# Optimization experiments

Measured on AMD Instinct MI355X. Metric: run time of the kernel, lower is better.

## Reference

```python
import jax, jax.numpy as jnp
import numpy as np

N, L, H, E = 4, 4096, 8, 64
CHUNK = 128  # chunk size for the blocked causal scan
EPS = 1e-6


def elu_feature_map(x):
    # phi(x) = elu(x) + 1 (default feature map of fast-transformers)
    return jax.nn.elu(x) + 1.0


def causal_dot_product(Q, K, V, chunk=CHUNK):
    """out[n,l,h,:] = sum_{s<=l} (Q[n,l,h,:].K[n,s,h,:]) * V[n,s,h,:].
    Chunked scan over the [E,M] KV state: O(N L H E M) without an [L,L] matrix."""
    n, l, h, e = Q.shape
    m = V.shape[-1]
    nc = l // chunk

    def to_chunks(x):
        # [n, l, h, d] -> [nc, n, h, chunk, d]
        return x.reshape(n, nc, chunk, h, x.shape[-1]).transpose(1, 0, 3, 2, 4)

    q, k, v = to_chunks(Q), to_chunks(K), to_chunks(V)
    tril = jnp.tril(jnp.ones((chunk, chunk), dtype=Q.dtype))

    def step(S, xs):  # S: [n, h, e, m] running sum of k v^T
        qc, kc, vc = xs  # [n, h, chunk, e/m]
        inter = jnp.einsum('nhce,nhem->nhcm', qc, S)
        attn = jnp.einsum('nhce,nhde->nhcd', qc, kc) * tril  # intra-chunk causal
        intra = jnp.einsum('nhcd,nhdm->nhcm', attn, vc)
        S = S + jnp.einsum('nhce,nhcm->nhem', kc, vc)
        return S, inter + intra

    S0 = jnp.zeros((n, h, e, m), dtype=Q.dtype)
    _, out = jax.lax.scan(step, S0, (q, k, v))  # [nc, n, h, chunk, m]
    return out.transpose(1, 0, 3, 2, 4).reshape(n, l, h, m)


def setup_inputs() -> dict:
    key = jax.random.key(0)
    k1, k2, k3 = jax.random.split(key, 3)
    return {
        'queries': jax.random.normal(k1, (N, L, H, E), jnp.float32),
        'keys': jax.random.normal(k2, (N, L, H, E), jnp.float32),
        'values': jax.random.normal(k3, (N, L, H, E), jnp.float32),
        'key_lengths': jnp.ones((N, L), jnp.float32),  # float length mask
    }


def reference(queries, keys, values, key_lengths):
    Q = elu_feature_map(queries)
    K = elu_feature_map(keys) * key_lengths[:, :, None, None]
    # denominator: Z[n,l,h] = 1 / (Q[n,l,h] . cumsum_s<=l K[n,s,h] + eps)
    Z = 1.0 / (jnp.einsum('nlhe,nlhe->nlh', Q, jnp.cumsum(K, axis=1)) + EPS)
    V_new = causal_dot_product(Q, K, values)
    return V_new * Z[:, :, :, None]
```

## Files before the change

kernel.cpp:

```cpp
#include <hip/hip_runtime.h>
#include <math.h>

#define NN 4
#define LL 4096
#define HH 8
#define EE 64
#define CHK 64
#define NCH (LL/CHK)
#define NG (NN*HH*NCH)
#define EPSF 1e-6f

typedef float f32x4 __attribute__((ext_vector_type(4)));
typedef __bf16 bf16x8 __attribute__((ext_vector_type(8)));

__device__ __forceinline__ float phi_map(float x) {
  return x > 0.0f ? x + 1.0f : __expf(x);
}

#define MFMA(a, b, c) __builtin_amdgcn_mfma_f32_16x16x32_bf16((a), (b), (c), 0, 0, 0)

__device__ __forceinline__ int swz64(int row, int d) {
  return row * 64 + (d & 7) + 8 * ((d >> 3) ^ ((row >> 2) & 7));
}
__device__ __forceinline__ int frag64(int row, int blk) {
  return row * 64 + 8 * (blk ^ ((row >> 2) & 7));
}

__global__ __launch_bounds__(256) void k_chunksums(
    const float* __restrict__ Kg, const float* __restrict__ Vg,
    const float* __restrict__ KLg, __bf16* __restrict__ ScG, __bf16* __restrict__ KscG)
{
  __shared__ __bf16 sKt[4096];
  __shared__ __bf16 sVt[4096];
  const int g = blockIdx.x;
  const int c = g % NCH;
  const int nh = g / NCH;
  const int h = nh % HH;
  const int n = nh / HH;
  const int l0 = c * CHK;
  const int t = threadIdx.x;

  #pragma unroll
  for (int it = 0; it < 4; ++it) {
    int f = t + 256 * it;
    int d = f >> 4;
    int c4 = (f & 15) << 2;
    size_t gb = (((size_t)n * LL + (size_t)(l0 + d)) * HH + h) * EE + c4;
    float4 kk = *(const float4*)(Kg + gb);
    float4 vv = *(const float4*)(Vg + gb);
    float klr = KLg[n * LL + l0 + d];
    float ka[4] = {phi_map(kk.x) * klr, phi_map(kk.y) * klr,
                   phi_map(kk.z) * klr, phi_map(kk.w) * klr};
    float va[4] = {vv.x, vv.y, vv.z, vv.w};
    #pragma unroll
    for (int j = 0; j < 4; ++j) {
      sKt[swz64(c4 + j, d)] = (__bf16)ka[j];
      sVt[swz64(c4 + j, d)] = (__bf16)va[j];
    }
  }
  __syncthreads();

  const int w = t >> 6;
  const int lane = t & 63;
  const int lg = lane >> 4;
  const int li = lane & 15;

  bf16x8 aV[2];
  #pragma unroll
  for (int ks = 0; ks < 2; ++ks)
    aV[ks] = *(const bf16x8*)&sVt[frag64(16 * w + li, 4 * ks + lg)];

  bf16x8 ones;
  #pragma unroll
  for (int i = 0; i < 8; ++i) ones[i] = (__bf16)1.0f;

  f32x4 acc[4], accK[4];
  #pragma unroll
  for (int nt = 0; nt < 4; ++nt) {
    acc[nt] = (f32x4){0.f, 0.f, 0.f, 0.f};
    accK[nt] = (f32x4){0.f, 0.f, 0.f, 0.f};
  }

  #pragma unroll
  for (int nt = 0; nt < 4; ++nt) {
    #pragma unroll
    for (int ks = 0; ks < 2; ++ks) {
      bf16x8 b = *(const bf16x8*)&sKt[frag64(li + 16 * nt, 4 * ks + lg)];
      acc[nt] = MFMA(aV[ks], b, acc[nt]);
      if (w == 0) accK[nt] = MFMA(ones, b, accK[nt]);
    }
  }

  __bf16* sp = ScG + (size_t)g * 4096;
  #pragma unroll
  for (int nt = 0; nt < 4; ++nt)
    #pragma unroll
    for (int reg = 0; reg < 4; ++reg)
      sp[(16 * w + 4 * lg + reg) * 64 + li + 16 * nt] = (__bf16)acc[nt][reg];

  if (w == 0 && lg == 0) {
    #pragma unroll
    for (int nt = 0; nt < 4; ++nt)
      KscG[(size_t)g * 64 + li + 16 * nt] = (__bf16)accK[nt][0];
  }
}

__global__ __launch_bounds__(256) void k_prefix(
    __bf16* __restrict__ Sc, __bf16* __restrict__ Ksc)
{
  const int bid = blockIdx.x;
  const int t = threadIdx.x;
  if (bid < NN * HH * 16) {
    const int nh = bid >> 4;
    const int strip = bid & 15;
    const int entry = strip * 256 + t;
    __bf16 v[NCH];
    #pragma unroll
    for (int c = 0; c < NCH; ++c)
      v[c] = Sc[((size_t)(nh * NCH + c) << 12) + entry];
    float run = 0.0f;
    #pragma unroll
    for (int c = 0; c < NCH; ++c) {
      Sc[((size_t)(nh * NCH + c) << 12) + entry] = (__bf16)run;
      run += (float)v[c];
    }
  } else {
    const int idx = (bid - NN * HH * 16) * 256 + t;
    const int nh = idx >> 6;
    const int e = idx & 63;
    __bf16 v[NCH];
    #pragma unroll
    for (int c = 0; c < NCH; ++c)
      v[c] = Ksc[((size_t)(nh * NCH + c) << 6) + e];
    float run = 0.0f;
    #pragma unroll
    for (int c = 0; c < NCH; ++c) {
      Ksc[((size_t)(nh * NCH + c) << 6) + e] = (__bf16)run;
      run += (float)v[c];
    }
  }
}

__global__ __launch_bounds__(256, 6) void k_pass2(
    const float* __restrict__ Qg, const float* __restrict__ Kg,
    const float* __restrict__ Vg, const float* __restrict__ KLg,
    const __bf16* __restrict__ Sp, const __bf16* __restrict__ Ksp,
    float* __restrict__ Og)
{
  __shared__ __bf16 sK[64][72];
  __shared__ __bf16 sVt[4096];
  __shared__ __bf16 sU[4608];

  const int g = blockIdx.x;
  const int c = g % NCH;
  const int nh = g / NCH;
  const int h = nh % HH;
  const int n = nh / HH;
  const int t = threadIdx.x;
  const int w = t >> 6;
  const int lane = t & 63;
  const int lg = lane >> 4;
  const int li = lane & 15;
  const int l0 = c * CHK;

  {
    const bf16x8* sp8 = (const bf16x8*)(Sp + (size_t)g * 4096);
    bf16x8 s0 = sp8[2 * t];
    bf16x8 s1 = sp8[2 * t + 1];
    int m = t >> 2;
    int e0 = (t & 3) * 16;
    *(bf16x8*)&sU[m * 72 + e0] = s0;
    *(bf16x8*)&sU[m * 72 + e0 + 8] = s1;
  }

  #pragma unroll
  for (int it = 0; it < 4; ++it) {
    int f = t + 256 * it;
    int rr = f >> 4;
    int c4 = (f & 15) << 2;
    size_t gb = (((size_t)n * LL + (size_t)(l0 + rr)) * HH + h) * EE + c4;
    float4 kk = *(const float4*)(Kg + gb);
    float4 vv = *(const float4*)(Vg + gb);
    float klr = KLg[n * LL + l0 + rr];
    __bf16* kd = &sK[rr][c4];
    kd[0] = (__bf16)(phi_map(kk.x) * klr); kd[1] = (__bf16)(phi_map(kk.y) * klr);
    kd[2] = (__bf16)(phi_map(kk.z) * klr); kd[3] = (__bf16)(phi_map(kk.w) * klr);
    float va[4] = {vv.x, vv.y, vv.z, vv.w};
    #pragma unroll
    for (int j = 0; j < 4; ++j)
      sVt[swz64(c4 + j, rr)] = (__bf16)va[j];
  }

  const int arow = 16 * w + li;
  const float* qrow = Qg + (((size_t)n * LL + (size_t)(l0 + arow)) * HH + h) * EE;
  float4 q0 = *(const float4*)(qrow + 8 * lg);
  float4 q1 = *(const float4*)(qrow + 8 * lg + 4);
  float4 q2 = *(const float4*)(qrow + 32 + 8 * lg);
  float4 q3 = *(const float4*)(qrow + 32 + 8 * lg + 4);
  bf16x8 aQ0, aQ1;
  aQ0[0] = (__bf16)phi_map(q0.x); aQ0[1] = (__bf16)phi_map(q0.y);
  aQ0[2] = (__bf16)phi_map(q0.z); aQ0[3] = (__bf16)phi_map(q0.w);
  aQ0[4] = (__bf16)phi_map(q1.x); aQ0[5] = (__bf16)phi_map(q1.y);
  aQ0[6] = (__bf16)phi_map(q1.z); aQ0[7] = (__bf16)phi_map(q1.w);
  aQ1[0] = (__bf16)phi_map(q2.x); aQ1[1] = (__bf16)phi_map(q2.y);
  aQ1[2] = (__bf16)phi_map(q2.z); aQ1[3] = (__bf16)phi_map(q2.w);
  aQ1[4] = (__bf16)phi_map(q3.x); aQ1[5] = (__bf16)phi_map(q3.y);
  aQ1[6] = (__bf16)phi_map(q3.z); aQ1[7] = (__bf16)phi_map(q3.w);

  const __bf16* kb = Ksp + (size_t)g * 64;
  bf16x8 ks0 = *(const bf16x8*)(kb + 8 * lg);
  bf16x8 ks1 = *(const bf16x8*)(kb + 32 + 8 * lg);

  __syncthreads();

  f32x4 acc[4];
  #pragma unroll
  for (int nt = 0; nt < 4; ++nt) acc[nt] = (f32x4){0.f, 0.f, 0.f, 0.f};
  #pragma unroll
  for (int nt = 0; nt < 4; ++nt) {
    bf16x8 b0 = *(const bf16x8*)&sU[(li + 16 * nt) * 72 + 8 * lg];
    bf16x8 b1 = *(const bf16x8*)&sU[(li + 16 * nt) * 72 + 32 + 8 * lg];
    acc[nt] = MFMA(aQ0, b0, acc[nt]);
    acc[nt] = MFMA(aQ1, b1, acc[nt]);
  }

  float dv = 0.0f;
  #pragma unroll
  for (int i = 0; i < 8; ++i) {
    dv += (float)aQ0[i] * (float)ks0[i];
    dv += (float)aQ1[i] * (float)ks1[i];
  }
  dv += __shfl_xor(dv, 16);
  dv += __shfl_xor(dv, 32);
  float den[4];
  #pragma unroll
  for (int reg = 0; reg < 4; ++reg) den[reg] = __shfl(dv, 4 * lg + reg);

  __syncthreads();

  float rs[4] = {0.f, 0.f, 0.f, 0.f};
  #pragma unroll
  for (int nt = 0; nt < 4; ++nt) {
    f32x4 at2 = (f32x4){0.f, 0.f, 0.f, 0.f};
    if (nt <= w) {
      bf16x8 b0 = *(const bf16x8*)&sK[li + 16 * nt][8 * lg];
      bf16x8 b1 = *(const bf16x8*)&sK[li + 16 * nt][32 + 8 * lg];
      at2 = MFMA(aQ0, b0, at2);
      at2 = MFMA(aQ1, b1, at2);
    }
    #pragma unroll
    for (int reg = 0; reg < 4; ++reg) {
      int row = 16 * w + 4 * lg + reg;
      int col = li + 16 * nt;
      float av = (col <= row) ? at2[reg] : 0.0f;
      rs[reg] += av;
      sU[w * 1152 + (4 * lg + reg) * 72 + col] = (__bf16)av;
    }
  }

  {
    bf16x8 aA0 = *(const bf16x8*)&sU[w * 1152 + li * 72 + 8 * lg];
    bf16x8 aA1 = aA0;
    if (w >= 2) aA1 = *(const bf16x8*)&sU[w * 1152 + li * 72 + 32 + 8 * lg];
    #pragma unroll
    for (int nt = 0; nt < 4; ++nt) {
      bf16x8 bv0 = *(const bf16x8*)&sVt[frag64(li + 16 * nt, lg)];
      acc[nt] = MFMA(aA0, bv0, acc[nt]);
      if (w >= 2) {
        bf16x8 bv1 = *(const bf16x8*)&sVt[frag64(li + 16 * nt, 4 + lg)];
        acc[nt] = MFMA(aA1, bv1, acc[nt]);
      }
    }
  }

  #pragma unroll
  for (int reg = 0; reg < 4; ++reg) {
    float v = rs[reg];
    v += __shfl_xor(v, 1);
    v += __shfl_xor(v, 2);
    v += __shfl_xor(v, 4);
    v += __shfl_xor(v, 8);
    rs[reg] = v;
  }

  #pragma unroll
  for (int reg = 0; reg < 4; ++reg) {
    float inv = 1.0f / (den[reg] + rs[reg] + EPSF);
    int row = l0 + 16 * w + 4 * lg + reg;
    size_t ob = (((size_t)n * LL + row) * HH + h) * EE + li;
    #pragma unroll
    for (int nt = 0; nt < 4; ++nt)
      Og[ob + 16 * nt] = acc[nt][reg] * inv;
  }
}

extern "C" void kernel_launch(void* const* d_in, const int* in_sizes, int n_in,
                              void* d_out, int out_size, void* d_ws, size_t ws_size,
                              hipStream_t stream) {
  const float* Qg  = (const float*)d_in[0];
  const float* Kg  = (const float*)d_in[1];
  const float* Vg  = (const float*)d_in[2];
  const float* KLg = (const float*)d_in[3];
  float* Og = (float*)d_out;

  __bf16* Sc  = (__bf16*)d_ws;
  __bf16* Ksc = (__bf16*)((char*)d_ws + (size_t)NG * 4096 * 2);

  hipLaunchKernelGGL(k_chunksums, dim3(NG), dim3(256), 0, stream, Kg, Vg, KLg, Sc, Ksc);
  hipLaunchKernelGGL(k_prefix, dim3(NN*HH*16 + 8), dim3(256), 0, stream, Sc, Ksc);
  hipLaunchKernelGGL(k_pass2, dim3(NG), dim3(256), 0, stream, Qg, Kg, Vg, KLg, Sc, Ksc, Og);
}
```

Before: 51.34 us.

## Process four chunks per block with in-block state carry and register prefetch

Each block now handles a super-chunk of four 64-row chunks instead of one. Inside a block the KV state is carried forward with MFMA updates, so the inter-block prefix scan works on a quarter as many state entries. Global loads of the next chunk are prefetched into registers and staged into double-buffered shared memory while the current chunk computes. In exchange, blocks run a serial dependency chain, the grid is four times smaller (512 blocks), and each block uses more shared memory and registers.

```diff
diff --git a/kernel.cpp b/kernel.cpp
--- a/kernel.cpp
+++ b/kernel.cpp
@@ -6,8 +6,12 @@
 #define HH 8
 #define EE 64
 #define CHK 64
-#define NCH (LL/CHK)
-#define NG (NN*HH*NCH)
+#define GSUP 4
+#define SUPC (CHK*GSUP)
+#define NSUP (LL/SUPC)
+#define NH (NN*HH)
+#define NBLK (NH*NSUP)
+#define NCH64 (LL/CHK)
 #define EPSF 1e-6f
 
 typedef float f32x4 __attribute__((ext_vector_type(4)));
@@ -26,134 +30,34 @@
   return row * 64 + 8 * (blk ^ ((row >> 2) & 7));
 }
 
-__global__ __launch_bounds__(256) void k_chunksums(
+#define K1_ISSUE(J, BUF) { \
+  const int l0i = (sc * GSUP + (J)) * CHK; \
+  _Pragma("unroll") for (int it = 0; it < 4; ++it) { \
+    int f = t + 256 * it; int d = f >> 4; int c4 = (f & 15) << 2; \
+    size_t gb = (((size_t)n * LL + (size_t)(l0i + d)) * HH + h) * EE + c4; \
+    pk[BUF][it] = *(const float4*)(Kg + gb); \
+    pv[BUF][it] = *(const float4*)(Vg + gb); \
+    pl[BUF][it] = KLg[n * LL + l0i + d]; } }
+
+#define K1_STAGE(BUF) { \
+  _Pragma("unroll") for (int it = 0; it < 4; ++it) { \
+    int f = t + 256 * it; int d = f >> 4; int c4 = (f & 15) << 2; \
+    float klr = pl[BUF][it]; float4 kk = pk[BUF][it]; float4 vv = pv[BUF][it]; \
+    float ka[4] = {phi_map(kk.x) * klr, phi_map(kk.y) * klr, phi_map(kk.z) * klr, phi_map(kk.w) * klr}; \
+    float va[4] = {vv.x, vv.y, vv.z, vv.w}; \
+    _Pragma("unroll") for (int jj = 0; jj < 4; ++jj) { \
+      sKt[BUF][swz64(c4 + jj, d)] = (__bf16)ka[jj]; \
+      sVt[BUF][swz64(c4 + jj, d)] = (__bf16)va[jj]; } } }
+
+__global__ __launch_bounds__(256, 2) void k_chunksums(
     const float* __restrict__ Kg, const float* __restrict__ Vg,
     const float* __restrict__ KLg, __bf16* __restrict__ ScG, __bf16* __restrict__ KscG)
 {
-  __shared__ __bf16 sKt[4096];
-  __shared__ __bf16 sVt[4096];
+  __shared__ __bf16 sKt[2][4096];
+  __shared__ __bf16 sVt[2][4096];
   const int g = blockIdx.x;
-  const int c = g % NCH;
-  const int nh = g / NCH;
-  const int h = nh % HH;
-  const int n = nh / HH;
-  const int l0 = c * CHK;
-  const int t = threadIdx.x;
-
-  #pragma unroll
-  for (int it = 0; it < 4; ++it) {
-    int f = t + 256 * it;
-    int d = f >> 4;
-    int c4 = (f & 15) << 2;
-    size_t gb = (((size_t)n * LL + (size_t)(l0 + d)) * HH + h) * EE + c4;
-    float4 kk = *(const float4*)(Kg + gb);
-    float4 vv = *(const float4*)(Vg + gb);
-    float klr = KLg[n * LL + l0 + d];
-    float ka[4] = {phi_map(kk.x) * klr, phi_map(kk.y) * klr,
-                   phi_map(kk.z) * klr, phi_map(kk.w) * klr};
-    float va[4] = {vv.x, vv.y, vv.z, vv.w};
-    #pragma unroll
-    for (int j = 0; j < 4; ++j) {
-      sKt[swz64(c4 + j, d)] = (__bf16)ka[j];
-      sVt[swz64(c4 + j, d)] = (__bf16)va[j];
-    }
-  }
-  __syncthreads();
-
-  const int w = t >> 6;
-  const int lane = t & 63;
-  const int lg = lane >> 4;
-  const int li = lane & 15;
-
-  bf16x8 aV[2];
-  #pragma unroll
-  for (int ks = 0; ks < 2; ++ks)
-    aV[ks] = *(const bf16x8*)&sVt[frag64(16 * w + li, 4 * ks + lg)];
-
-  bf16x8 ones;
-  #pragma unroll
-  for (int i = 0; i < 8; ++i) ones[i] = (__bf16)1.0f;
-
-  f32x4 acc[4], accK[4];
-  #pragma unroll
-  for (int nt = 0; nt < 4; ++nt) {
-    acc[nt] = (f32x4){0.f, 0.f, 0.f, 0.f};
-    accK[nt] = (f32x4){0.f, 0.f, 0.f, 0.f};
-  }
-
-  #pragma unroll
-  for (int nt = 0; nt < 4; ++nt) {
-    #pragma unroll
-    for (int ks = 0; ks < 2; ++ks) {
-      bf16x8 b = *(const bf16x8*)&sKt[frag64(li + 16 * nt, 4 * ks + lg)];
-      acc[nt] = MFMA(aV[ks], b, acc[nt]);
-      if (w == 0) accK[nt] = MFMA(ones, b, accK[nt]);
-    }
-  }
-
-  __bf16* sp = ScG + (size_t)g * 4096;
-  #pragma unroll
-  for (int nt = 0; nt < 4; ++nt)
-    #pragma unroll
-    for (int reg = 0; reg < 4; ++reg)
-      sp[(16 * w + 4 * lg + reg) * 64 + li + 16 * nt] = (__bf16)acc[nt][reg];
-
-  if (w == 0 && lg == 0) {
-    #pragma unroll
-    for (int nt = 0; nt < 4; ++nt)
-      KscG[(size_t)g * 64 + li + 16 * nt] = (__bf16)accK[nt][0];
-  }
-}
-
-__global__ __launch_bounds__(256) void k_prefix(
-    __bf16* __restrict__ Sc, __bf16* __restrict__ Ksc)
-{
-  const int bid = blockIdx.x;
-  const int t = threadIdx.x;
-  if (bid < NN * HH * 16) {
-    const int nh = bid >> 4;
-    const int strip = bid & 15;
-    const int entry = strip * 256 + t;
-    __bf16 v[NCH];
-    #pragma unroll
-    for (int c = 0; c < NCH; ++c)
-      v[c] = Sc[((size_t)(nh * NCH + c) << 12) + entry];
-    float run = 0.0f;
-    #pragma unroll
-    for (int c = 0; c < NCH; ++c) {
-      Sc[((size_t)(nh * NCH + c) << 12) + entry] = (__bf16)run;
-      run += (float)v[c];
-    }
-  } else {
-    const int idx = (bid - NN * HH * 16) * 256 + t;
-    const int nh = idx >> 6;
-    const int e = idx & 63;
-    __bf16 v[NCH];
-    #pragma unroll
-    for (int c = 0; c < NCH; ++c)
-      v[c] = Ksc[((size_t)(nh * NCH + c) << 6) + e];
-    float run = 0.0f;
-    #pragma unroll
-    for (int c = 0; c < NCH; ++c) {
-      Ksc[((size_t)(nh * NCH + c) << 6) + e] = (__bf16)run;
-      run += (float)v[c];
-    }
-  }
-}
-
-__global__ __launch_bounds__(256, 6) void k_pass2(
-    const float* __restrict__ Qg, const float* __restrict__ Kg,
-    const float* __restrict__ Vg, const float* __restrict__ KLg,
-    const __bf16* __restrict__ Sp, const __bf16* __restrict__ Ksp,
-    float* __restrict__ Og)
-{
-  __shared__ __bf16 sK[64][72];
-  __shared__ __bf16 sVt[4096];
-  __shared__ __bf16 sU[4608];
-
-  const int g = blockIdx.x;
-  const int c = g % NCH;
-  const int nh = g / NCH;
+  const int sc = g % NSUP;
+  const int nh = g / NSUP;
   const int h = nh % HH;
   const int n = nh / HH;
   const int t = threadIdx.x;
@@ -161,7 +65,147 @@
   const int lane = t & 63;
   const int lg = lane >> 4;
   const int li = lane & 15;
-  const int l0 = c * CHK;
+
+  float4 pk[2][4], pv[2][4];
+  float pl[2][4];
+
+  K1_ISSUE(0, 0);
+  K1_STAGE(0);
+
+  f32x4 acc[4];
+  #pragma unroll
+  for (int nt = 0; nt < 4; ++nt) acc[nt] = (f32x4){0.f, 0.f, 0.f, 0.f};
+
+  bf16x8 ones;
+  #pragma unroll
+  for (int i = 0; i < 8; ++i) ones[i] = (__bf16)1.0f;
+
+  #pragma unroll
+  for (int j = 0; j < GSUP; ++j) {
+    if (j + 1 < GSUP) K1_ISSUE(j + 1, (j + 1) & 1);
+    __syncthreads();
+
+    bf16x8 aV0 = *(const bf16x8*)&sVt[j & 1][frag64(16 * w + li, lg)];
+    bf16x8 aV1 = *(const bf16x8*)&sVt[j & 1][frag64(16 * w + li, 4 + lg)];
+
+    f32x4 accK[4];
+    #pragma unroll
+    for (int nt = 0; nt < 4; ++nt) accK[nt] = (f32x4){0.f, 0.f, 0.f, 0.f};
+
+    #pragma unroll
+    for (int nt = 0; nt < 4; ++nt) {
+      bf16x8 b0 = *(const bf16x8*)&sKt[j & 1][frag64(li + 16 * nt, lg)];
+      bf16x8 b1 = *(const bf16x8*)&sKt[j & 1][frag64(li + 16 * nt, 4 + lg)];
+      acc[nt] = MFMA(aV0, b0, acc[nt]);
+      acc[nt] = MFMA(aV1, b1, acc[nt]);
+      if (w == 0) {
+        accK[nt] = MFMA(ones, b0, accK[nt]);
+        accK[nt] = MFMA(ones, b1, accK[nt]);
+      }
+    }
+    if (w == 0 && lg == 0) {
+      #pragma unroll
+      for (int nt = 0; nt < 4; ++nt)
+        KscG[(size_t)(g * GSUP + j) * 64 + li + 16 * nt] = (__bf16)accK[nt][0];
+    }
+    if (j + 1 < GSUP) K1_STAGE((j + 1) & 1);
+  }
+
+  __bf16* sp = ScG + (size_t)g * 4096;
+  #pragma unroll
+  for (int nt = 0; nt < 4; ++nt)
+    #pragma unroll
+    for (int reg = 0; reg < 4; ++reg)
+      sp[(16 * w + 4 * lg + reg) * 64 + li + 16 * nt] = (__bf16)acc[nt][reg];
+}
+
+__global__ __launch_bounds__(256) void k_prefix(
+    __bf16* __restrict__ Sc, __bf16* __restrict__ Ksc)
+{
+  const int bid = blockIdx.x;
+  const int t = threadIdx.x;
+  if (bid < NH * 16) {
+    const int nh = bid >> 4;
+    const int strip = bid & 15;
+    const int entry = strip * 256 + t;
+    __bf16 v[NSUP];
+    #pragma unroll
+    for (int c = 0; c < NSUP; ++c)
+      v[c] = Sc[((size_t)(nh * NSUP + c) << 12) + entry];
+    float run = 0.0f;
+    #pragma unroll
+    for (int c = 0; c < NSUP; ++c) {
+      Sc[((size_t)(nh * NSUP + c) << 12) + entry] = (__bf16)run;
+      run += (float)v[c];
+    }
+  } else {
+    const int idx = (bid - NH * 16) * 256 + t;
+    const int nh = idx >> 6;
+    const int e = idx & 63;
+    __bf16 v[NCH64];
+    #pragma unroll
+    for (int c = 0; c < NCH64; ++c)
+      v[c] = Ksc[((size_t)(nh * NCH64 + c) << 6) + e];
+    float run = 0.0f;
+    #pragma unroll
+    for (int c = 0; c < NCH64; ++c) {
+      Ksc[((size_t)(nh * NCH64 + c) << 6) + e] = (__bf16)run;
+      run += (float)v[c];
+    }
+  }
+}
+
+#define P2_ISSUE(CC, BUF) { \
+  const int l0i = (sc * GSUP + (CC)) * CHK; \
+  _Pragma("unroll") for (int it = 0; it < 4; ++it) { \
+    int f = t + 256 * it; int rr = f >> 4; int c4 = (f & 15) << 2; \
+    size_t gb = (((size_t)n * LL + (size_t)(l0i + rr)) * HH + h) * EE + c4; \
+    pk[BUF][it] = *(const float4*)(Kg + gb); \
+    pv[BUF][it] = *(const float4*)(Vg + gb); \
+    pl[BUF][it] = KLg[n * LL + l0i + rr]; } \
+  { const float* qrow = Qg + (((size_t)n * LL + (size_t)(l0i + arow)) * HH + h) * EE; \
+    pq[BUF][0] = *(const float4*)(qrow + 8 * lg); \
+    pq[BUF][1] = *(const float4*)(qrow + 8 * lg + 4); \
+    pq[BUF][2] = *(const float4*)(qrow + 32 + 8 * lg); \
+    pq[BUF][3] = *(const float4*)(qrow + 32 + 8 * lg + 4); } }
+
+#define P2_STAGE(BUF) { \
+  _Pragma("unroll") for (int it = 0; it < 4; ++it) { \
+    int f = t + 256 * it; int rr = f >> 4; int c4 = (f & 15) << 2; \
+    float klr = pl[BUF][it]; float4 kk = pk[BUF][it]; float4 vv = pv[BUF][it]; \
+    float ka[4] = {phi_map(kk.x) * klr, phi_map(kk.y) * klr, phi_map(kk.z) * klr, phi_map(kk.w) * klr}; \
+    float va[4] = {vv.x, vv.y, vv.z, vv.w}; \
+    __bf16* kd = &sK[BUF][rr][c4]; \
+    kd[0] = (__bf16)ka[0]; kd[1] = (__bf16)ka[1]; kd[2] = (__bf16)ka[2]; kd[3] = (__bf16)ka[3]; \
+    _Pragma("unroll") for (int jj = 0; jj < 4; ++jj) { \
+      sKt[BUF][swz64(c4 + jj, rr)] = (__bf16)ka[jj]; \
+      sVt[BUF][swz64(c4 + jj, rr)] = (__bf16)va[jj]; } } }
+
+__global__ __launch_bounds__(256, 2) void k_pass2(
+    const float* __restrict__ Qg, const float* __restrict__ Kg,
+    const float* __restrict__ Vg, const float* __restrict__ KLg,
+    const __bf16* __restrict__ Sp, const __bf16* __restrict__ Ksp,
+    float* __restrict__ Og)
+{
+  __shared__ __bf16 sK[2][64][72];
+  __shared__ __bf16 sKt[2][4096];
+  __shared__ __bf16 sVt[2][4096];
+  __shared__ __bf16 sU[4608];
+
+  const int g = blockIdx.x;
+  const int sc = g % NSUP;
+  const int nh = g / NSUP;
+  const int h = nh % HH;
+  const int n = nh / HH;
+  const int t = threadIdx.x;
+  const int w = t >> 6;
+  const int lane = t & 63;
+  const int lg = lane >> 4;
+  const int li = lane & 15;
+  const int arow = 16 * w + li;
+
+  float4 pk[2][4], pv[2][4], pq[2][4];
+  float pl[2][4];
 
   {
     const bf16x8* sp8 = (const bf16x8*)(Sp + (size_t)g * 4096);
@@ -173,124 +217,145 @@
     *(bf16x8*)&sU[m * 72 + e0 + 8] = s1;
   }
 
-  #pragma unroll
-  for (int it = 0; it < 4; ++it) {
-    int f = t + 256 * it;
-    int rr = f >> 4;
-    int c4 = (f & 15) << 2;
-    size_t gb = (((size_t)n * LL + (size_t)(l0 + rr)) * HH + h) * EE + c4;
-    float4 kk = *(const float4*)(Kg + gb);
-    float4 vv = *(const float4*)(Vg + gb);
-    float klr = KLg[n * LL + l0 + rr];
-    __bf16* kd = &sK[rr][c4];
-    kd[0] = (__bf16)(phi_map(kk.x) * klr); kd[1] = (__bf16)(phi_map(kk.y) * klr);
-    kd[2] = (__bf16)(phi_map(kk.z) * klr); kd[3] = (__bf16)(phi_map(kk.w) * klr);
-    float va[4] = {vv.x, vv.y, vv.z, vv.w};
-    #pragma unroll
-    for (int j = 0; j < 4; ++j)
-      sVt[swz64(c4 + j, rr)] = (__bf16)va[j];
-  }
-
-  const int arow = 16 * w + li;
-  const float* qrow = Qg + (((size_t)n * LL + (size_t)(l0 + arow)) * HH + h) * EE;
-  float4 q0 = *(const float4*)(qrow + 8 * lg);
-  float4 q1 = *(const float4*)(qrow + 8 * lg + 4);
-  float4 q2 = *(const float4*)(qrow + 32 + 8 * lg);
-  float4 q3 = *(const float4*)(qrow + 32 + 8 * lg + 4);
-  bf16x8 aQ0, aQ1;
-  aQ0[0] = (__bf16)phi_map(q0.x); aQ0[1] = (__bf16)phi_map(q0.y);
-  aQ0[2] = (__bf16)phi_map(q0.z); aQ0[3] = (__bf16)phi_map(q0.w);
-  aQ0[4] = (__bf16)phi_map(q1.x); aQ0[5] = (__bf16)phi_map(q1.y);
-  aQ0[6] = (__bf16)phi_map(q1.z); aQ0[7] = (__bf16)phi_map(q1.w);
-  aQ1[0] = (__bf16)phi_map(q2.x); aQ1[1] = (__bf16)phi_map(q2.y);
-  aQ1[2] = (__bf16)phi_map(q2.z); aQ1[3] = (__bf16)phi_map(q2.w);
-  aQ1[4] = (__bf16)phi_map(q3.x); aQ1[5] = (__bf16)phi_map(q3.y);
-  aQ1[6] = (__bf16)phi_map(q3.z); aQ1[7] = (__bf16)phi_map(q3.w);
-
-  const __bf16* kb = Ksp + (size_t)g * 64;
-  bf16x8 ks0 = *(const bf16x8*)(kb + 8 * lg);
-  bf16x8 ks1 = *(const bf16x8*)(kb + 32 + 8 * lg);
-
-  __syncthreads();
-
-  f32x4 acc[4];
-  #pragma unroll
-  for (int nt = 0; nt < 4; ++nt) acc[nt] = (f32x4){0.f, 0.f, 0.f, 0.f};
-  #pragma unroll
-  for (int nt = 0; nt < 4; ++nt) {
-    bf16x8 b0 = *(const bf16x8*)&sU[(li + 16 * nt) * 72 + 8 * lg];
-    bf16x8 b1 = *(const bf16x8*)&sU[(li + 16 * nt) * 72 + 32 + 8 * lg];
-    acc[nt] = MFMA(aQ0, b0, acc[nt]);
-    acc[nt] = MFMA(aQ1, b1, acc[nt]);
-  }
-
-  float dv = 0.0f;
-  #pragma unroll
-  for (int i = 0; i < 8; ++i) {
-    dv += (float)aQ0[i] * (float)ks0[i];
-    dv += (float)aQ1[i] * (float)ks1[i];
-  }
-  dv += __shfl_xor(dv, 16);
-  dv += __shfl_xor(dv, 32);
-  float den[4];
-  #pragma unroll
-  for (int reg = 0; reg < 4; ++reg) den[reg] = __shfl(dv, 4 * lg + reg);
-
-  __syncthreads();
-
-  float rs[4] = {0.f, 0.f, 0.f, 0.f};
-  #pragma unroll
-  for (int nt = 0; nt < 4; ++nt) {
-    f32x4 at2 = (f32x4){0.f, 0.f, 0.f, 0.f};
-    if (nt <= w) {
-      bf16x8 b0 = *(const bf16x8*)&sK[li + 16 * nt][8 * lg];
-      bf16x8 b1 = *(const bf16x8*)&sK[li + 16 * nt][32 + 8 * lg];
-      at2 = MFMA(aQ0, b0, at2);
-      at2 = MFMA(aQ1, b1, at2);
-    }
+  P2_ISSUE(0, 0);
+  P2_STAGE(0);
+
+  float bSp[4][4];
+  f32x4 accS[4];
+  #pragma unroll
+  for (int nt = 0; nt < 4; ++nt) accS[nt] = (f32x4){0.f, 0.f, 0.f, 0.f};
+
+  #pragma unroll
+  for (int cc = 0; cc < GSUP; ++cc) {
+    __syncthreads();
+
+    if (cc == 0) {
+      #pragma unroll
+      for (int nt = 0; nt < 4; ++nt)
+        #pragma unroll
+        for (int reg = 0; reg < 4; ++reg)
+          bSp[nt][reg] = (float)sU[(16 * w + 4 * lg + reg) * 72 + 16 * nt + li];
+    }
+
+    if (cc + 1 < GSUP) P2_ISSUE(cc + 1, (cc + 1) & 1);
+
+    bf16x8 aQ0, aQ1;
+    {
+      float4 q0 = pq[cc & 1][0], q1 = pq[cc & 1][1], q2 = pq[cc & 1][2], q3 = pq[cc & 1][3];
+      aQ0[0] = (__bf16)phi_map(q0.x); aQ0[1] = (__bf16)phi_map(q0.y);
+      aQ0[2] = (__bf16)phi_map(q0.z); aQ0[3] = (__bf16)phi_map(q0.w);
+      aQ0[4] = (__bf16)phi_map(q1.x); aQ0[5] = (__bf16)phi_map(q1.y);
+      aQ0[6] = (__bf16)phi_map(q1.z); aQ0[7] = (__bf16)phi_map(q1.w);
+      aQ1[0] = (__bf16)phi_map(q2.x); aQ1[1] = (__bf16)phi_map(q2.y);
+      aQ1[2] = (__bf16)phi_map(q2.z); aQ1[3] = (__bf16)phi_map(q2.w);
+      aQ1[4] = (__bf16)phi_map(q3.x); aQ1[5] = (__bf16)phi_map(q3.y);
+      aQ1[6] = (__bf16)phi_map(q3.z); aQ1[7] = (__bf16)phi_map(q3.w);
+    }
+
+    const __bf16* kb = Ksp + (size_t)(g * GSUP + cc) * 64;
+    bf16x8 ks0 = *(const bf16x8*)(kb + 8 * lg);
+    bf16x8 ks1 = *(const bf16x8*)(kb + 32 + 8 * lg);
+
+    f32x4 acc[4];
+    #pragma unroll
+    for (int nt = 0; nt < 4; ++nt) acc[nt] = (f32x4){0.f, 0.f, 0.f, 0.f};
+    #pragma unroll
+    for (int nt = 0; nt < 4; ++nt) {
+      bf16x8 b0 = *(const bf16x8*)&sU[(li + 16 * nt) * 72 + 8 * lg];
+      bf16x8 b1 = *(const bf16x8*)&sU[(li + 16 * nt) * 72 + 32 + 8 * lg];
+      acc[nt] = MFMA(aQ0, b0, acc[nt]);
+      acc[nt] = MFMA(aQ1, b1, acc[nt]);
+    }
+
+    float dv = 0.0f;
+    #pragma unroll
+    for (int i = 0; i < 8; ++i) {
+      dv += (float)aQ0[i] * (float)ks0[i];
+      dv += (float)aQ1[i] * (float)ks1[i];
+    }
+    dv += __shfl_xor(dv, 16);
+    dv += __shfl_xor(dv, 32);
+    float den[4];
+    #pragma unroll
+    for (int reg = 0; reg < 4; ++reg) den[reg] = __shfl(dv, 4 * lg + reg);
+
+    __syncthreads();
+
+    float rs[4] = {0.f, 0.f, 0.f, 0.f};
+    #pragma unroll
+    for (int nt = 0; nt < 4; ++nt) {
+      f32x4 at2 = (f32x4){0.f, 0.f, 0.f, 0.f};
+      if (nt <= w) {
+        bf16x8 b0 = *(const bf16x8*)&sK[cc & 1][li + 16 * nt][8 * lg];
+        bf16x8 b1 = *(const bf16x8*)&sK[cc & 1][li + 16 * nt][32 + 8 * lg];
+        at2 = MFMA(aQ0, b0, at2);
+        at2 = MFMA(aQ1, b1, at2);
+      }
+      #pragma unroll
+      for (int reg = 0; reg < 4; ++reg) {
+        int row = 16 * w + 4 * lg + reg;
+        int col = li + 16 * nt;
+        float av = (col <= row) ? at2[reg] : 0.0f;
+        rs[reg] += av;
+        sU[w * 1152 + (4 * lg + reg) * 72 + col] = (__bf16)av;
+      }
+    }
+
+    {
+      bf16x8 aA0 = *(const bf16x8*)&sU[w * 1152 + li * 72 + 8 * lg];
+      bf16x8 aA1 = aA0;
+      if (w >= 2) aA1 = *(const bf16x8*)&sU[w * 1152 + li * 72 + 32 + 8 * lg];
+      #pragma unroll
+      for (int nt = 0; nt < 4; ++nt) {
+        bf16x8 bv0 = *(const bf16x8*)&sVt[cc & 1][frag64(li + 16 * nt, lg)];
+        acc[nt] = MFMA(aA0, bv0, acc[nt]);
+        if (w >= 2) {
+          bf16x8 bv1 = *(const bf16x8*)&sVt[cc & 1][frag64(li + 16 * nt, 4 + lg)];
+          acc[nt] = MFMA(aA1, bv1, acc[nt]);
+        }
+      }
+    }
+
     #pragma unroll
     for (int reg = 0; reg < 4; ++reg) {
-      int row = 16 * w + 4 * lg + reg;
-      int col = li + 16 * nt;
-      float av = (col <= row) ? at2[reg] : 0.0f;
-      rs[reg] += av;
-      sU[w * 1152 + (4 * lg + reg) * 72 + col] = (__bf16)av;
-    }
-  }
-
-  {
-    bf16x8 aA0 = *(const bf16x8*)&sU[w * 1152 + li * 72 + 8 * lg];
-    bf16x8 aA1 = aA0;
-    if (w >= 2) aA1 = *(const bf16x8*)&sU[w * 1152 + li * 72 + 32 + 8 * lg];
-    #pragma unroll
-    for (int nt = 0; nt < 4; ++nt) {
-      bf16x8 bv0 = *(const bf16x8*)&sVt[frag64(li + 16 * nt, lg)];
-      acc[nt] = MFMA(aA0, bv0, acc[nt]);
-      if (w >= 2) {
-        bf16x8 bv1 = *(const bf16x8*)&sVt[frag64(li + 16 * nt, 4 + lg)];
-        acc[nt] = MFMA(aA1, bv1, acc[nt]);
-      }
-    }
-  }
-
-  #pragma unroll
-  for (int reg = 0; reg < 4; ++reg) {
-    float v = rs[reg];
-    v += __shfl_xor(v, 1);
-    v += __shfl_xor(v, 2);
-    v += __shfl_xor(v, 4);
-    v += __shfl_xor(v, 8);
-    rs[reg] = v;
-  }
-
-  #pragma unroll
-  for (int reg = 0; reg < 4; ++reg) {
-    float inv = 1.0f / (den[reg] + rs[reg] + EPSF);
-    int row = l0 + 16 * w + 4 * lg + reg;
-    size_t ob = (((size_t)n * LL + row) * HH + h) * EE + li;
-    #pragma unroll
-    for (int nt = 0; nt < 4; ++nt)
-      Og[ob + 16 * nt] = acc[nt][reg] * inv;
+      float v = rs[reg];
+      v += __shfl_xor(v, 1);
+      v += __shfl_xor(v, 2);
+      v += __shfl_xor(v, 4);
+      v += __shfl_xor(v, 8);
+      rs[reg] = v;
+    }
+
+    const int l0 = (sc * GSUP + cc) * CHK;
+    #pragma unroll
+    for (int reg = 0; reg < 4; ++reg) {
+      float inv = 1.0f / (den[reg] + rs[reg] + EPSF);
+      int row = l0 + 16 * w + 4 * lg + reg;
+      size_t ob = (((size_t)n * LL + row) * HH + h) * EE + li;
+      #pragma unroll
+      for (int nt = 0; nt < 4; ++nt)
+        Og[ob + 16 * nt] = acc[nt][reg] * inv;
+    }
+
+    if (cc + 1 < GSUP) {
+      bf16x8 aV0 = *(const bf16x8*)&sVt[cc & 1][frag64(16 * w + li, lg)];
+      bf16x8 aV1 = *(const bf16x8*)&sVt[cc & 1][frag64(16 * w + li, 4 + lg)];
+      #pragma unroll
+      for (int nt = 0; nt < 4; ++nt) {
+        bf16x8 b0 = *(const bf16x8*)&sKt[cc & 1][frag64(li + 16 * nt, lg)];
+        bf16x8 b1 = *(const bf16x8*)&sKt[cc & 1][frag64(li + 16 * nt, 4 + lg)];
+        accS[nt] = MFMA(aV0, b0, accS[nt]);
+        accS[nt] = MFMA(aV1, b1, accS[nt]);
+      }
+      #pragma unroll
+      for (int nt = 0; nt < 4; ++nt)
+        #pragma unroll
+        for (int reg = 0; reg < 4; ++reg)
+          sU[(16 * w + 4 * lg + reg) * 72 + 16 * nt + li] =
+            (__bf16)(bSp[nt][reg] + accS[nt][reg]);
+
+      P2_STAGE((cc + 1) & 1);
+    }
   }
 }
 
@@ -304,9 +369,9 @@
   float* Og = (float*)d_out;
 
   __bf16* Sc  = (__bf16*)d_ws;
-  __bf16* Ksc = (__bf16*)((char*)d_ws + (size_t)NG * 4096 * 2);
-
-  hipLaunchKernelGGL(k_chunksums, dim3(NG), dim3(256), 0, stream, Kg, Vg, KLg, Sc, Ksc);
-  hipLaunchKernelGGL(k_prefix, dim3(NN*HH*16 + 8), dim3(256), 0, stream, Sc, Ksc);
-  hipLaunchKernelGGL(k_pass2, dim3(NG), dim3(256), 0, stream, Qg, Kg, Vg, KLg, Sc, Ksc, Og);
-}
+  __bf16* Ksc = (__bf16*)((char*)d_ws + (size_t)NBLK * 4096 * 2);
+
+  hipLaunchKernelGGL(k_chunksums, dim3(NBLK), dim3(256), 0, stream, Kg, Vg, KLg, Sc, Ksc);
+  hipLaunchKernelGGL(k_prefix, dim3(NH * 16 + 8), dim3(256), 0, stream, Sc, Ksc);
+  hipLaunchKernelGGL(k_pass2, dim3(NBLK), dim3(256), 0, stream, Qg, Kg, Vg, KLg, Sc, Ksc, Og);
+}
```

After: 48.10 us. 1.07x faster.
